# Kernel optimization log

Hardware: AMD Instinct MI355X
Metric: run time of the kernel (lower is better)

## Reference

```python
import jax, jax.numpy as jnp
import numpy as np

BIG_K, SMALL_K = 13, 3
NK = -(-BIG_K // SMALL_K)  # 5
NUM_PATHS = 3
BN_EPS = 1e-5


def _shifts():
    mid = BIG_K // 2
    pad = SMALL_K - 1
    return [-(mid - i * SMALL_K - pad) for i in range(NK)]  # [-4,-1,2,5,8]


def _conv1x1(x, w):
    return jax.lax.conv_general_dilated(
        x, w, window_strides=(1, 1), padding='VALID',
        dimension_numbers=('NCHW', 'OIHW', 'NCHW'))


def _dwconv3x3(x, w, groups):
    # x: (b, groups, h, w); w: (groups, 1, 3, 3)
    return jax.lax.conv_general_dilated(
        x, w, window_strides=(1, 1), padding=[(1, 1), (1, 1)],
        dimension_numbers=('NCHW', 'OIHW', 'NCHW'),
        feature_group_count=groups)


def setup_inputs() -> dict:
    key = jax.random.key(0)
    ks = jax.random.split(key, 8)
    b, c1, c2, h, w = 16, 256, 256, 64, 64
    return {
        'x': jax.random.normal(ks[0], (b, c1, h, w), jnp.float32),
        'w_expand': jax.random.normal(ks[1], (c2 * NK, c1, 1, 1), jnp.float32) * 0.05,
        'w_path': jax.random.normal(ks[2], (NUM_PATHS, NK, c2, 1, 3, 3), jnp.float32) * 0.1,
        'w_mix': jax.random.normal(ks[3], (c2, c2, 1, 1), jnp.float32) * 0.05,
        'bn_gamma': jnp.ones((c2,), jnp.float32),
        'bn_beta': jnp.zeros((c2,), jnp.float32),
        'bn_mean': jnp.zeros((c2,), jnp.float32),
        'bn_var': jnp.ones((c2,), jnp.float32),
    }


def reference(x, w_expand, w_path, w_mix, bn_gamma, bn_beta, bn_mean, bn_var):
    b, c1, h, w = x.shape
    c2 = w_mix.shape[0]
    # 1) channel expand: c1 -> c2*nk (1x1 conv, big GEMM)
    x_exp = _conv1x1(x, w_expand)                      # (b, c2*NK, h, w)
    x_r = x_exp.reshape(b, c2, NK, h, w)
    # 2) roll each shift group; conv is linear in kernel, so summing over the
    #    3 paths of depthwise weights gives identical math to summing outputs.
    shifts = _shifts()
    rolled = jnp.stack(
        [jnp.roll(x_r[:, :, k], (shifts[k], shifts[k]), axis=(2, 3)) for k in range(NK)],
        axis=2)                                        # (b, c2, NK, h, w)
    rolled_flat = rolled.reshape(b, c2 * NK, h, w)      # channel layout: c2-major, nk-minor
    w_eff = jnp.sum(w_path, axis=0)                     # (NK, c2, 1, 3, 3)
    w_flat = jnp.transpose(w_eff, (1, 0, 2, 3, 4)).reshape(c2 * NK, 1, 3, 3)
    conv_out = _dwconv3x3(rolled_flat, w_flat, groups=c2 * NK)
    merged = conv_out.reshape(b, c2, NK, h, w).sum(axis=2)  # sum over shifts (paths already folded)
    # 3) channel mix + BN (inference) + SiLU
    out = _conv1x1(merged, w_mix)
    inv = jax.lax.rsqrt(bn_var + BN_EPS)
    out = (out - bn_mean[None, :, None, None]) * (bn_gamma * inv)[None, :, None, None] + bn_beta[None, :, None, None]
    return out * jax.nn.sigmoid(out)  # SiLU
```

## Files before the change

kernel.cpp:

```cpp
#include <hip/hip_runtime.h>
#include <hip/hip_bf16.h>
#include <math.h>

#define NB   16
#define C1   256
#define C2   256
#define NK   5
#define NEXP (C2 * NK)
#define HW   4096

typedef __attribute__((ext_vector_type(8))) short bf16x8;
typedef __attribute__((ext_vector_type(4))) float f32x4;

#define GLOAD_LDS16(g, l) __builtin_amdgcn_global_load_lds( \
    (const __attribute__((address_space(1))) void*)(g), \
    (__attribute__((address_space(3))) void*)(l), 16, 0, 0)

__device__ __forceinline__ int bswz(int n, int kByte) {
    return n * 64 + (kByte ^ (((n >> 1) & 3) << 4));
}

__global__ void weff_kernel(const float* __restrict__ w_path, float* __restrict__ weff) {
    int idx = blockIdx.x * 256 + threadIdx.x;
    if (idx >= NK * C2 * 9) return;
    float s = 0.f;
    #pragma unroll
    for (int p = 0; p < 3; ++p)
        s += w_path[(long)p * NK * C2 * 9 + idx];
    weff[idx] = s;
}

__global__ void cvt_bf16_kernel(const float* __restrict__ in, __hip_bfloat16* __restrict__ out, int n) {
    int i = blockIdx.x * 256 + threadIdx.x;
    if (i < n) out[i] = __float2bfloat16(in[i]);
}

template <bool FP32B, bool OUT_BF16>
__global__ __launch_bounds__(256)
void gemm_mfma_kernel(const __hip_bfloat16* __restrict__ A,
                      const void* __restrict__ B_all,
                      void* __restrict__ C_all, int M, int N, int K,
                      long bStrideB, long bStrideC, int bOffB, int bOffC,
                      const float* __restrict__ bn_gamma, const float* __restrict__ bn_beta,
                      const float* __restrict__ bn_mean, const float* __restrict__ bn_var) {
    __shared__ __align__(16) short As[128 * 32];
    __shared__ __align__(16) short Bs[128 * 32];
    const int z = blockIdx.z;
    const int n0 = blockIdx.x * 128;
    const int m0 = blockIdx.y * 128;
    const int t = threadIdx.x;
    const int lane = t & 63;
    const int wid = t >> 6;
    const int wr = wid >> 1, wc = wid & 1;
    const int lr = lane & 15, lg = lane >> 4;
    const int sr = t >> 2;
    const int sc = (t & 3) * 8;

    const __hip_bfloat16* aP0 = &A[(long)(m0 + sr) * K + sc];
    const __hip_bfloat16* aP1 = &A[(long)(m0 + 64 + sr) * K + sc];
    short* aD0 = &As[sr * 32 + sc];
    short* aD1 = &As[(64 + sr) * 32 + sc];

    const int bn = t & 127;
    const int kg = t >> 7;
    const float* Bf = (const float*)B_all + (long)(bOffB + z) * bStrideB + n0 + bn;
    const short* Bh = (const short*)B_all + (long)(bOffB + z) * bStrideB + n0 + bn;
    char* bD0 = (char*)Bs + bswz(bn, kg * 32);
    char* bD1 = (char*)Bs + bswz(bn, kg * 32 + 16);

    int bOff[4];
    #pragma unroll
    for (int i = 0; i < 4; ++i)
        bOff[i] = bswz(wc * 64 + i * 16 + lr, lg * 16);

    f32x4 acc[4][4];
    #pragma unroll
    for (int i = 0; i < 4; ++i)
        #pragma unroll
        for (int j = 0; j < 4; ++j)
            acc[i][j] = (f32x4){0.f, 0.f, 0.f, 0.f};

    for (int k0 = 0; k0 < K; k0 += 32) {
        bf16x8 pk0, pk1;
        #pragma unroll
        for (int i = 0; i < 8; ++i) {
            if constexpr (FP32B) {
                float v0 = Bf[(long)(k0 + kg * 16 + i) * N];
                float v1 = Bf[(long)(k0 + kg * 16 + 8 + i) * N];
                __hip_bfloat16 h0 = __float2bfloat16(v0);
                __hip_bfloat16 h1 = __float2bfloat16(v1);
                pk0[i] = *reinterpret_cast<short*>(&h0);
                pk1[i] = *reinterpret_cast<short*>(&h1);
            } else {
                pk0[i] = Bh[(long)(k0 + kg * 16 + i) * N];
                pk1[i] = Bh[(long)(k0 + kg * 16 + 8 + i) * N];
            }
        }
        __syncthreads();
        GLOAD_LDS16(aP0 + k0, aD0);
        GLOAD_LDS16(aP1 + k0, aD1);
        *(bf16x8*)bD0 = pk0;
        *(bf16x8*)bD1 = pk1;
        __syncthreads();
        bf16x8 af[4], bfr[4];
        #pragma unroll
        for (int i = 0; i < 4; ++i) {
            af[i]  = *(const bf16x8*)&As[(wr * 64 + i * 16 + lr) * 32 + lg * 8];
            bfr[i] = *(const bf16x8*)((char*)Bs + bOff[i]);
        }
        #pragma unroll
        for (int i = 0; i < 4; ++i)
            #pragma unroll
            for (int j = 0; j < 4; ++j)
                acc[i][j] = __builtin_amdgcn_mfma_f32_16x16x32_bf16(af[i], bfr[j], acc[i][j], 0, 0, 0);
    }

    if constexpr (OUT_BF16) {
        __hip_bfloat16* C = (__hip_bfloat16*)C_all + (long)(bOffC + z) * bStrideC;
        #pragma unroll
        for (int i = 0; i < 4; ++i) {
            #pragma unroll
            for (int r = 0; r < 4; ++r) {
                long row = m0 + wr * 64 + i * 16 + lg * 4 + r;
                #pragma unroll
                for (int j = 0; j < 4; ++j)
                    C[row * N + n0 + wc * 64 + j * 16 + lr] = __float2bfloat16(acc[i][j][r]);
            }
        }
    } else {
        float* C = (float*)C_all + (long)(bOffC + z) * bStrideC;
        #pragma unroll
        for (int i = 0; i < 4; ++i) {
            #pragma unroll
            for (int r = 0; r < 4; ++r) {
                int row = m0 + wr * 64 + i * 16 + lg * 4 + r;
                float scale = bn_gamma[row] * rsqrtf(bn_var[row] + 1e-5f);
                float mn = bn_mean[row], bt = bn_beta[row];
                #pragma unroll
                for (int j = 0; j < 4; ++j) {
                    float v = (acc[i][j][r] - mn) * scale + bt;
                    C[(long)row * N + n0 + wc * 64 + j * 16 + lr] = v / (1.0f + __expf(-v));
                }
            }
        }
    }
}

__global__ __launch_bounds__(256)
void shift_dw_kernel(const __hip_bfloat16* __restrict__ xexp,
                     const float* __restrict__ weff,
                     __hip_bfloat16* __restrict__ merged) {
    __shared__ __align__(16) __hip_bfloat16 sd[NK * 34 * 64];
    const int t  = threadIdx.x;
    const int r0 = blockIdx.x * 32;
    const int c  = blockIdx.y;
    const int z  = blockIdx.z;
    const int shifts[NK] = {-4, -1, 2, 5, 8};
    const __hip_bfloat16* base = xexp + ((long)z * NEXP + (long)c * NK) * HW;

    for (int idx = t; idx < NK * 34 * 8; idx += 256) {
        int k   = idx / (34 * 8);
        int rem = idx - k * (34 * 8);
        int rr  = rem >> 3, ch = (rem & 7) * 8;
        int grow = (r0 - 1 + rr - shifts[k]) & 63;
        *(bf16x8*)&sd[(k * 34 + rr) * 64 + ch] =
            *(const bf16x8*)(base + (long)k * HW + grow * 64 + ch);
    }
    __syncthreads();

    const int j  = t & 63;
    const int ty = t >> 6;
    const int pbase = ty * 8;
    const bool topEdge = (r0 == 0)  && (ty == 0);
    const bool botEdge = (r0 == 32) && (ty == 3);

    float2 acc[4];
    #pragma unroll
    for (int i = 0; i < 4; ++i) acc[i] = (float2){0.f, 0.f};

    #pragma unroll
    for (int k = 0; k < NK; ++k) {
        const int s = shifts[k];
        const int cL = (j - 1 - s) & 63;
        const int cC = (j - s) & 63;
        const int cR = (j + 1 - s) & 63;
        const float* wp = &weff[((long)k * C2 + c) * 9];
        float w[9];
        #pragma unroll
        for (int i = 0; i < 9; ++i) w[i] = wp[i];
        if (j == 0)  { w[0] = 0.f; w[3] = 0.f; w[6] = 0.f; }
        if (j == 63) { w[2] = 0.f; w[5] = 0.f; w[8] = 0.f; }
        const __hip_bfloat16* pl = &sd[k * 34 * 64];

        float vL[4], vC[4], vR[4];
        #pragma unroll
        for (int w4 = 0; w4 < 4; ++w4) {
            vL[w4] = __bfloat162float(pl[(pbase + w4) * 64 + cL]);
            vC[w4] = __bfloat162float(pl[(pbase + w4) * 64 + cC]);
            vR[w4] = __bfloat162float(pl[(pbase + w4) * 64 + cR]);
        }
        if (topEdge) { vL[0] = 0.f; vC[0] = 0.f; vR[0] = 0.f; }

        #pragma unroll
        for (int pr = 0; pr < 4; ++pr) {
            #pragma unroll
            for (int u = 0; u < 3; ++u) {
                const int wi  = (2 * pr + u) & 3;
                const int wi2 = (2 * pr + u + 1) & 3;
                acc[pr].x += w[u*3+0] * vL[wi]  + w[u*3+1] * vC[wi]  + w[u*3+2] * vR[wi];
                acc[pr].y += w[u*3+0] * vL[wi2] + w[u*3+1] * vC[wi2] + w[u*3+2] * vR[wi2];
            }
            if (pr < 3) {
                const int na = (2 * pr) & 3, nb = (2 * pr + 1) & 3;
                const int ra = pbase + 2 * pr + 4, rb = pbase + 2 * pr + 5;
                vL[na] = __bfloat162float(pl[ra * 64 + cL]);
                vC[na] = __bfloat162float(pl[ra * 64 + cC]);
                vR[na] = __bfloat162float(pl[ra * 64 + cR]);
                vL[nb] = __bfloat162float(pl[rb * 64 + cL]);
                vC[nb] = __bfloat162float(pl[rb * 64 + cC]);
                vR[nb] = __bfloat162float(pl[rb * 64 + cR]);
                if (botEdge && pr == 2) { vL[nb] = 0.f; vC[nb] = 0.f; vR[nb] = 0.f; }
            }
        }
    }

    long outb = ((long)z * C2 + c) * HW + (long)(r0 + ty * 8) * 64 + j;
    #pragma unroll
    for (int pr = 0; pr < 4; ++pr) {
        merged[outb + (long)(2 * pr) * 64]     = __float2bfloat16(acc[pr].x);
        merged[outb + (long)(2 * pr + 1) * 64] = __float2bfloat16(acc[pr].y);
    }
}

extern "C" void kernel_launch(void* const* d_in, const int* in_sizes, int n_in,
                              void* d_out, int out_size, void* d_ws, size_t ws_size,
                              hipStream_t stream) {
    const float* x        = (const float*)d_in[0];
    const float* w_expand = (const float*)d_in[1];
    const float* w_path   = (const float*)d_in[2];
    const float* w_mix    = (const float*)d_in[3];
    const float* bn_gamma = (const float*)d_in[4];
    const float* bn_beta  = (const float*)d_in[5];
    const float* bn_mean  = (const float*)d_in[6];
    const float* bn_var   = (const float*)d_in[7];

    char* ws = (char*)d_ws;
    float* weff             = (float*)ws;
    __hip_bfloat16* wexp_bf = (__hip_bfloat16*)(ws + 65536);
    __hip_bfloat16* wmix_bf = (__hip_bfloat16*)(ws + 65536 + 655360);
    const size_t head = 1 << 20;

    const size_t xe_per = (size_t)NEXP * HW * 2;
    const size_t mg_per = (size_t)C2 * HW * 2;
    const size_t per_b = xe_per + mg_per;

    int g = 1;
    if (ws_size > head + per_b) {
        size_t fit = (ws_size - head) / per_b;
        g = (int)(fit < NB ? fit : NB);
        if (g < 1) g = 1;
    }

    char* p = ws + head;
    __hip_bfloat16* xexp   = (__hip_bfloat16*)p; p += (size_t)g * xe_per;
    __hip_bfloat16* merged = (__hip_bfloat16*)p;

    weff_kernel<<<(NK * C2 * 9 + 255) / 256, 256, 0, stream>>>(w_path, weff);
    cvt_bf16_kernel<<<(NEXP * C1 + 255) / 256, 256, 0, stream>>>(w_expand, wexp_bf, NEXP * C1);
    cvt_bf16_kernel<<<(C2 * C2 + 255) / 256, 256, 0, stream>>>(w_mix, wmix_bf, C2 * C2);

    for (int b0 = 0; b0 < NB; b0 += g) {
        int gb = (NB - b0) < g ? (NB - b0) : g;
        gemm_mfma_kernel<true, true><<<dim3(HW / 128, NEXP / 128, gb), 256, 0, stream>>>(
            wexp_bf, x, xexp, NEXP, HW, C1,
            (long)C1 * HW, (long)NEXP * HW, b0, 0,
            nullptr, nullptr, nullptr, nullptr);
        shift_dw_kernel<<<dim3(2, C2, gb), 256, 0, stream>>>(xexp, weff, merged);
        gemm_mfma_kernel<false, false><<<dim3(HW / 128, C2 / 128, gb), 256, 0, stream>>>(
            wmix_bf, merged, d_out, C2, HW, C2,
            (long)C2 * HW, (long)C2 * HW, 0, b0,
            bn_gamma, bn_beta, bn_mean, bn_var);
    }
}
```

Measured before the change: 248.2 us.

## Double-buffer GEMM LDS tiles, vectorize B loads and transpose MFMA output stores

The MFMA GEMM now keeps two LDS buffers so the next K-tile's global loads (A through direct-to-LDS, B through registers) are issued while the current tile is computed, needing one barrier per iteration instead of two. B is read with vectorized float4/bf16x8 loads and packed as k-pairs, and both tiles use an XOR swizzle to avoid LDS bank conflicts. The MFMA operands are swapped so each lane owns four consecutive columns, which lets the epilogue write short4/float4 vectors instead of scattered scalars. The cost is double the LDS footprint, which may lower occupancy, plus more complex swizzle indexing that has to stay correct.

```diff
diff --git a/kernel.cpp b/kernel.cpp
--- a/kernel.cpp
+++ b/kernel.cpp
@@ -16,8 +16,10 @@
     (const __attribute__((address_space(1))) void*)(g), \
     (__attribute__((address_space(3))) void*)(l), 16, 0, 0)
 
-__device__ __forceinline__ int bswz(int n, int kByte) {
-    return n * 64 + (kByte ^ (((n >> 1) & 3) << 4));
+__device__ __forceinline__ int swzkey(int r) { return ((r >> 1) & 3) ^ ((r >> 3) & 3); }
+
+__device__ __forceinline__ unsigned short bfbits(float v) {
+    return __builtin_bit_cast(unsigned short, __float2bfloat16(v));
 }
 
 __global__ void weff_kernel(const float* __restrict__ w_path, float* __restrict__ weff) {
@@ -43,8 +45,8 @@
                       long bStrideB, long bStrideC, int bOffB, int bOffC,
                       const float* __restrict__ bn_gamma, const float* __restrict__ bn_beta,
                       const float* __restrict__ bn_mean, const float* __restrict__ bn_var) {
-    __shared__ __align__(16) short As[128 * 32];
-    __shared__ __align__(16) short Bs[128 * 32];
+    __shared__ __align__(16) short As[2][128 * 32];
+    __shared__ __align__(16) short Bs[2][128 * 32];
     const int z = blockIdx.z;
     const int n0 = blockIdx.x * 128;
     const int m0 = blockIdx.y * 128;
@@ -53,25 +55,52 @@
     const int wid = t >> 6;
     const int wr = wid >> 1, wc = wid & 1;
     const int lr = lane & 15, lg = lane >> 4;
-    const int sr = t >> 2;
-    const int sc = (t & 3) * 8;
-
-    const __hip_bfloat16* aP0 = &A[(long)(m0 + sr) * K + sc];
-    const __hip_bfloat16* aP1 = &A[(long)(m0 + 64 + sr) * K + sc];
-    short* aD0 = &As[sr * 32 + sc];
-    short* aD1 = &As[(64 + sr) * 32 + sc];
-
-    const int bn = t & 127;
-    const int kg = t >> 7;
-    const float* Bf = (const float*)B_all + (long)(bOffB + z) * bStrideB + n0 + bn;
-    const short* Bh = (const short*)B_all + (long)(bOffB + z) * bStrideB + n0 + bn;
-    char* bD0 = (char*)Bs + bswz(bn, kg * 32);
-    char* bD1 = (char*)Bs + bswz(bn, kg * 32 + 16);
-
-    int bOff[4];
-    #pragma unroll
-    for (int i = 0; i < 4; ++i)
-        bOff[i] = bswz(wc * 64 + i * 16 + lr, lg * 16);
+
+    const int arow = t >> 2, achk = t & 3;
+    const int akey = swzkey(arow);
+    const __hip_bfloat16* aS0 = A + (long)(m0 + arow) * K + (achk ^ akey) * 8;
+    const __hip_bfloat16* aS1 = A + (long)(m0 + 64 + arow) * K + (achk ^ akey) * 8;
+
+    const int pr = (t >> 4) & 15;
+    const int ng = t & 15;
+    const char* Bbase = (const char*)B_all + (long)(bOffB + z) * bStrideB * (FP32B ? 4 : 2);
+
+    int bwoff[8];
+    #pragma unroll
+    for (int jj = 0; jj < 8; ++jj) {
+        int n = ng * 8 + jj;
+        bwoff[jj] = n * 64 + (((pr >> 2) ^ swzkey(n)) << 4) + (pr & 3) * 4;
+    }
+    int aroff[4], broff[4];
+    #pragma unroll
+    for (int i = 0; i < 4; ++i) {
+        int r = wr * 64 + i * 16 + lr;
+        aroff[i] = r * 64 + ((lg ^ swzkey(r)) << 4);
+        int n = wc * 64 + i * 16 + lr;
+        broff[i] = n * 64 + ((lg ^ swzkey(n)) << 4);
+    }
+
+    auto loadB = [&](int k0, unsigned u[8]) {
+        if constexpr (FP32B) {
+            const float* p0 = (const float*)Bbase + (long)(k0 + 2 * pr) * N + n0 + ng * 8;
+            const float* p1 = p0 + N;
+            float4 x0 = ((const float4*)p0)[0], x1 = ((const float4*)p0)[1];
+            float4 y0 = ((const float4*)p1)[0], y1 = ((const float4*)p1)[1];
+            float xs[8] = {x0.x, x0.y, x0.z, x0.w, x1.x, x1.y, x1.z, x1.w};
+            float ys[8] = {y0.x, y0.y, y0.z, y0.w, y1.x, y1.y, y1.z, y1.w};
+            #pragma unroll
+            for (int jj = 0; jj < 8; ++jj)
+                u[jj] = (unsigned)bfbits(xs[jj]) | ((unsigned)bfbits(ys[jj]) << 16);
+        } else {
+            const short* p0 = (const short*)Bbase + (long)(k0 + 2 * pr) * N + n0 + ng * 8;
+            bf16x8 r0 = *(const bf16x8*)p0;
+            bf16x8 r1 = *(const bf16x8*)(p0 + N);
+            #pragma unroll
+            for (int jj = 0; jj < 8; ++jj)
+                u[jj] = (unsigned)(unsigned short)r0[jj] |
+                        ((unsigned)(unsigned short)r1[jj] << 16);
+        }
+    };
 
     f32x4 acc[4][4];
     #pragma unroll
@@ -80,67 +109,82 @@
         for (int j = 0; j < 4; ++j)
             acc[i][j] = (f32x4){0.f, 0.f, 0.f, 0.f};
 
-    for (int k0 = 0; k0 < K; k0 += 32) {
-        bf16x8 pk0, pk1;
-        #pragma unroll
-        for (int i = 0; i < 8; ++i) {
-            if constexpr (FP32B) {
-                float v0 = Bf[(long)(k0 + kg * 16 + i) * N];
-                float v1 = Bf[(long)(k0 + kg * 16 + 8 + i) * N];
-                __hip_bfloat16 h0 = __float2bfloat16(v0);
-                __hip_bfloat16 h1 = __float2bfloat16(v1);
-                pk0[i] = *reinterpret_cast<short*>(&h0);
-                pk1[i] = *reinterpret_cast<short*>(&h1);
-            } else {
-                pk0[i] = Bh[(long)(k0 + kg * 16 + i) * N];
-                pk1[i] = Bh[(long)(k0 + kg * 16 + 8 + i) * N];
-            }
+    const int NT = K / 32;
+    unsigned ub[8];
+    loadB(0, ub);
+    GLOAD_LDS16(aS0, (char*)&As[0][0] + t * 16);
+    GLOAD_LDS16(aS1, (char*)&As[0][0] + 4096 + t * 16);
+    #pragma unroll
+    for (int jj = 0; jj < 8; ++jj)
+        *(unsigned*)((char*)&Bs[0][0] + bwoff[jj]) = ub[jj];
+    __syncthreads();
+
+    int buf = 0;
+    for (int it = 0; it < NT; ++it) {
+        unsigned un[8];
+        const bool more = (it + 1) < NT;
+        if (more) {
+            int k0 = (it + 1) * 32;
+            loadB(k0, un);
+            GLOAD_LDS16(aS0 + k0, (char*)&As[buf ^ 1][0] + t * 16);
+            GLOAD_LDS16(aS1 + k0, (char*)&As[buf ^ 1][0] + 4096 + t * 16);
+        }
+        bf16x8 af[4], bfr[4];
+        #pragma unroll
+        for (int i = 0; i < 4; ++i) {
+            af[i]  = *(const bf16x8*)((const char*)&As[buf][0] + aroff[i]);
+            bfr[i] = *(const bf16x8*)((const char*)&Bs[buf][0] + broff[i]);
+        }
+        #pragma unroll
+        for (int i = 0; i < 4; ++i)
+            #pragma unroll
+            for (int j = 0; j < 4; ++j)
+                acc[i][j] = __builtin_amdgcn_mfma_f32_16x16x32_bf16(bfr[j], af[i], acc[i][j], 0, 0, 0);
+        if (more) {
+            #pragma unroll
+            for (int jj = 0; jj < 8; ++jj)
+                *(unsigned*)((char*)&Bs[buf ^ 1][0] + bwoff[jj]) = un[jj];
         }
         __syncthreads();
-        GLOAD_LDS16(aP0 + k0, aD0);
-        GLOAD_LDS16(aP1 + k0, aD1);
-        *(bf16x8*)bD0 = pk0;
-        *(bf16x8*)bD1 = pk1;
-        __syncthreads();
-        bf16x8 af[4], bfr[4];
-        #pragma unroll
-        for (int i = 0; i < 4; ++i) {
-            af[i]  = *(const bf16x8*)&As[(wr * 64 + i * 16 + lr) * 32 + lg * 8];
-            bfr[i] = *(const bf16x8*)((char*)Bs + bOff[i]);
-        }
-        #pragma unroll
-        for (int i = 0; i < 4; ++i)
-            #pragma unroll
-            for (int j = 0; j < 4; ++j)
-                acc[i][j] = __builtin_amdgcn_mfma_f32_16x16x32_bf16(af[i], bfr[j], acc[i][j], 0, 0, 0);
+        buf ^= 1;
     }
 
     if constexpr (OUT_BF16) {
         __hip_bfloat16* C = (__hip_bfloat16*)C_all + (long)(bOffC + z) * bStrideC;
         #pragma unroll
         for (int i = 0; i < 4; ++i) {
-            #pragma unroll
-            for (int r = 0; r < 4; ++r) {
-                long row = m0 + wr * 64 + i * 16 + lg * 4 + r;
-                #pragma unroll
-                for (int j = 0; j < 4; ++j)
-                    C[row * N + n0 + wc * 64 + j * 16 + lr] = __float2bfloat16(acc[i][j][r]);
+            const int m = m0 + wr * 64 + i * 16 + lr;
+            #pragma unroll
+            for (int j = 0; j < 4; ++j) {
+                const long n = n0 + wc * 64 + j * 16 + lg * 4;
+                short4 sv;
+                sv.x = (short)bfbits(acc[i][j][0]);
+                sv.y = (short)bfbits(acc[i][j][1]);
+                sv.z = (short)bfbits(acc[i][j][2]);
+                sv.w = (short)bfbits(acc[i][j][3]);
+                *(short4*)(C + (long)m * N + n) = sv;
             }
         }
     } else {
         float* C = (float*)C_all + (long)(bOffC + z) * bStrideC;
         #pragma unroll
         for (int i = 0; i < 4; ++i) {
-            #pragma unroll
-            for (int r = 0; r < 4; ++r) {
-                int row = m0 + wr * 64 + i * 16 + lg * 4 + r;
-                float scale = bn_gamma[row] * rsqrtf(bn_var[row] + 1e-5f);
-                float mn = bn_mean[row], bt = bn_beta[row];
-                #pragma unroll
-                for (int j = 0; j < 4; ++j) {
-                    float v = (acc[i][j][r] - mn) * scale + bt;
-                    C[(long)row * N + n0 + wc * 64 + j * 16 + lr] = v / (1.0f + __expf(-v));
-                }
+            const int m = m0 + wr * 64 + i * 16 + lr;
+            const float scale = bn_gamma[m] * rsqrtf(bn_var[m] + 1e-5f);
+            const float mn = bn_mean[m], bt = bn_beta[m];
+            #pragma unroll
+            for (int j = 0; j < 4; ++j) {
+                const long n = n0 + wc * 64 + j * 16 + lg * 4;
+                float4 v;
+                float t0 = (acc[i][j][0] - mn) * scale + bt;
+                float t1 = (acc[i][j][1] - mn) * scale + bt;
+                float t2 = (acc[i][j][2] - mn) * scale + bt;
+                float t3 = (acc[i][j][3] - mn) * scale + bt;
+                v.x = t0 / (1.0f + __expf(-t0));
+                v.y = t1 / (1.0f + __expf(-t1));
+                v.z = t2 / (1.0f + __expf(-t2));
+                v.w = t3 / (1.0f + __expf(-t3));
+                *(float4*)(C + (long)m * N + n) = v;
             }
         }
     }
```

After: 265.6 us. 7.0% more time.

## Rewrite 1x1-conv GEMMs with register-resident weights and full-K B tile in LDS

Applied to the files above, without the earlier changes.

Replaces the K-looped 128x128 GEMM with a 512-thread kernel specialised for K=256. Each wave keeps its 32 weight rows for the whole K in registers, and the block stages the entire 256x128 activation tile in XOR-swizzled LDS once, so there is no per-k-step synchronisation. Operands are swapped so the output is vector-stored along N, using short4/float4 stores instead of scalar ones. This trades occupancy (64KB LDS, launch bounds of one block, heavy register use) for fewer barriers and wider stores.

```diff
diff --git a/kernel.cpp b/kernel.cpp
--- a/kernel.cpp
+++ b/kernel.cpp
@@ -12,12 +12,8 @@
 typedef __attribute__((ext_vector_type(8))) short bf16x8;
 typedef __attribute__((ext_vector_type(4))) float f32x4;
 
-#define GLOAD_LDS16(g, l) __builtin_amdgcn_global_load_lds( \
-    (const __attribute__((address_space(1))) void*)(g), \
-    (__attribute__((address_space(3))) void*)(l), 16, 0, 0)
-
-__device__ __forceinline__ int bswz(int n, int kByte) {
-    return n * 64 + (kByte ^ (((n >> 1) & 3) << 4));
+__device__ __forceinline__ unsigned short bfbits(float v) {
+    return __builtin_bit_cast(unsigned short, __float2bfloat16(v));
 }
 
 __global__ void weff_kernel(const float* __restrict__ w_path, float* __restrict__ weff) {
@@ -36,111 +32,113 @@
 }
 
 template <bool FP32B, bool OUT_BF16>
-__global__ __launch_bounds__(256)
-void gemm_mfma_kernel(const __hip_bfloat16* __restrict__ A,
-                      const void* __restrict__ B_all,
-                      void* __restrict__ C_all, int M, int N, int K,
-                      long bStrideB, long bStrideC, int bOffB, int bOffC,
-                      const float* __restrict__ bn_gamma, const float* __restrict__ bn_beta,
-                      const float* __restrict__ bn_mean, const float* __restrict__ bn_var) {
-    __shared__ __align__(16) short As[128 * 32];
-    __shared__ __align__(16) short Bs[128 * 32];
-    const int z = blockIdx.z;
+__global__ __launch_bounds__(512, 1)
+void ws_gemm_kernel(const __hip_bfloat16* __restrict__ A,
+                    const void* __restrict__ B_all,
+                    void* __restrict__ C_all,
+                    long bStrideB, long bStrideC, int bOffB, int bOffC,
+                    const float* __restrict__ bn_gamma, const float* __restrict__ bn_beta,
+                    const float* __restrict__ bn_mean, const float* __restrict__ bn_var) {
+    constexpr int KK = 256, NN = 4096;
+    __shared__ __align__(16) char Bs[128 * 512];
+    const int z  = blockIdx.z;
     const int n0 = blockIdx.x * 128;
-    const int m0 = blockIdx.y * 128;
-    const int t = threadIdx.x;
+    const int m0 = blockIdx.y * 256;
+    const int t  = threadIdx.x;
     const int lane = t & 63;
-    const int wid = t >> 6;
-    const int wr = wid >> 1, wc = wid & 1;
+    const int wv = t >> 6;
     const int lr = lane & 15, lg = lane >> 4;
-    const int sr = t >> 2;
-    const int sc = (t & 3) * 8;
-
-    const __hip_bfloat16* aP0 = &A[(long)(m0 + sr) * K + sc];
-    const __hip_bfloat16* aP1 = &A[(long)(m0 + 64 + sr) * K + sc];
-    short* aD0 = &As[sr * 32 + sc];
-    short* aD1 = &As[(64 + sr) * 32 + sc];
-
-    const int bn = t & 127;
-    const int kg = t >> 7;
-    const float* Bf = (const float*)B_all + (long)(bOffB + z) * bStrideB + n0 + bn;
-    const short* Bh = (const short*)B_all + (long)(bOffB + z) * bStrideB + n0 + bn;
-    char* bD0 = (char*)Bs + bswz(bn, kg * 32);
-    char* bD1 = (char*)Bs + bswz(bn, kg * 32 + 16);
-
-    int bOff[4];
-    #pragma unroll
-    for (int i = 0; i < 4; ++i)
-        bOff[i] = bswz(wc * 64 + i * 16 + lr, lg * 16);
-
-    f32x4 acc[4][4];
-    #pragma unroll
-    for (int i = 0; i < 4; ++i)
-        #pragma unroll
-        for (int j = 0; j < 4; ++j)
-            acc[i][j] = (f32x4){0.f, 0.f, 0.f, 0.f};
-
-    for (int k0 = 0; k0 < K; k0 += 32) {
-        bf16x8 pk0, pk1;
-        #pragma unroll
-        for (int i = 0; i < 8; ++i) {
-            if constexpr (FP32B) {
-                float v0 = Bf[(long)(k0 + kg * 16 + i) * N];
-                float v1 = Bf[(long)(k0 + kg * 16 + 8 + i) * N];
-                __hip_bfloat16 h0 = __float2bfloat16(v0);
-                __hip_bfloat16 h1 = __float2bfloat16(v1);
-                pk0[i] = *reinterpret_cast<short*>(&h0);
-                pk1[i] = *reinterpret_cast<short*>(&h1);
-            } else {
-                pk0[i] = Bh[(long)(k0 + kg * 16 + i) * N];
-                pk1[i] = Bh[(long)(k0 + kg * 16 + 8 + i) * N];
-            }
-        }
-        __syncthreads();
-        GLOAD_LDS16(aP0 + k0, aD0);
-        GLOAD_LDS16(aP1 + k0, aD1);
-        *(bf16x8*)bD0 = pk0;
-        *(bf16x8*)bD1 = pk1;
-        __syncthreads();
-        bf16x8 af[4], bfr[4];
-        #pragma unroll
-        for (int i = 0; i < 4; ++i) {
-            af[i]  = *(const bf16x8*)&As[(wr * 64 + i * 16 + lr) * 32 + lg * 8];
-            bfr[i] = *(const bf16x8*)((char*)Bs + bOff[i]);
-        }
-        #pragma unroll
-        for (int i = 0; i < 4; ++i)
-            #pragma unroll
-            for (int j = 0; j < 4; ++j)
-                acc[i][j] = __builtin_amdgcn_mfma_f32_16x16x32_bf16(af[i], bfr[j], acc[i][j], 0, 0, 0);
+
+    bf16x8 af[2][8];
+    const __hip_bfloat16* wp = A + (long)(m0 + wv * 32 + lr) * KK + lg * 8;
+    #pragma unroll
+    for (int s = 0; s < 2; ++s)
+        #pragma unroll
+        for (int ks = 0; ks < 8; ++ks)
+            af[s][ks] = *(const bf16x8*)(wp + (long)s * 16 * KK + ks * 32);
+
+    const int sn = t & 127;
+    const int kb = (t >> 7) * 64;
+    const int key = sn & 31;
+    const char* Bbase = (const char*)B_all + (long)(bOffB + z) * bStrideB * (FP32B ? 4 : 2);
+    #pragma unroll
+    for (int gq = 0; gq < 4; ++gq) {
+        unsigned u[8];
+        if constexpr (FP32B) {
+            const float* p = (const float*)Bbase + (long)(kb + gq * 16) * NN + n0 + sn;
+            #pragma unroll
+            for (int i = 0; i < 8; ++i) {
+                float v0 = p[(long)(2 * i) * NN];
+                float v1 = p[(long)(2 * i + 1) * NN];
+                u[i] = (unsigned)bfbits(v0) | ((unsigned)bfbits(v1) << 16);
+            }
+        } else {
+            const unsigned short* p = (const unsigned short*)Bbase + (long)(kb + gq * 16) * NN + n0 + sn;
+            #pragma unroll
+            for (int i = 0; i < 8; ++i)
+                u[i] = (unsigned)p[(long)(2 * i) * NN] |
+                       ((unsigned)p[(long)(2 * i + 1) * NN] << 16);
+        }
+        const int ch0 = kb / 8 + gq * 2;
+        *(uint4*)(Bs + sn * 512 + ((ch0 ^ key) * 16))       = *(uint4*)&u[0];
+        *(uint4*)(Bs + sn * 512 + (((ch0 + 1) ^ key) * 16)) = *(uint4*)&u[4];
+    }
+    __syncthreads();
+
+    f32x4 acc[2][8];
+    #pragma unroll
+    for (int s = 0; s < 2; ++s)
+        #pragma unroll
+        for (int j = 0; j < 8; ++j)
+            acc[s][j] = (f32x4){0.f, 0.f, 0.f, 0.f};
+
+    #pragma unroll
+    for (int ks = 0; ks < 8; ++ks) {
+        #pragma unroll
+        for (int j = 0; j < 8; ++j) {
+            const int n = j * 16 + lr;
+            bf16x8 bfr = *(const bf16x8*)(Bs + n * 512 + (((ks * 4 + lg) ^ (n & 31)) * 16));
+            acc[0][j] = __builtin_amdgcn_mfma_f32_16x16x32_bf16(bfr, af[0][ks], acc[0][j], 0, 0, 0);
+            acc[1][j] = __builtin_amdgcn_mfma_f32_16x16x32_bf16(bfr, af[1][ks], acc[1][j], 0, 0, 0);
+        }
     }
 
     if constexpr (OUT_BF16) {
         __hip_bfloat16* C = (__hip_bfloat16*)C_all + (long)(bOffC + z) * bStrideC;
         #pragma unroll
-        for (int i = 0; i < 4; ++i) {
-            #pragma unroll
-            for (int r = 0; r < 4; ++r) {
-                long row = m0 + wr * 64 + i * 16 + lg * 4 + r;
-                #pragma unroll
-                for (int j = 0; j < 4; ++j)
-                    C[row * N + n0 + wc * 64 + j * 16 + lr] = __float2bfloat16(acc[i][j][r]);
+        for (int s = 0; s < 2; ++s) {
+            const int m = m0 + wv * 32 + s * 16 + lr;
+            #pragma unroll
+            for (int j = 0; j < 8; ++j) {
+                const long n = n0 + j * 16 + lg * 4;
+                short4 sv;
+                sv.x = (short)bfbits(acc[s][j][0]);
+                sv.y = (short)bfbits(acc[s][j][1]);
+                sv.z = (short)bfbits(acc[s][j][2]);
+                sv.w = (short)bfbits(acc[s][j][3]);
+                *(short4*)(C + (long)m * NN + n) = sv;
             }
         }
     } else {
         float* C = (float*)C_all + (long)(bOffC + z) * bStrideC;
         #pragma unroll
-        for (int i = 0; i < 4; ++i) {
-            #pragma unroll
-            for (int r = 0; r < 4; ++r) {
-                int row = m0 + wr * 64 + i * 16 + lg * 4 + r;
-                float scale = bn_gamma[row] * rsqrtf(bn_var[row] + 1e-5f);
-                float mn = bn_mean[row], bt = bn_beta[row];
-                #pragma unroll
-                for (int j = 0; j < 4; ++j) {
-                    float v = (acc[i][j][r] - mn) * scale + bt;
-                    C[(long)row * N + n0 + wc * 64 + j * 16 + lr] = v / (1.0f + __expf(-v));
-                }
+        for (int s = 0; s < 2; ++s) {
+            const int m = m0 + wv * 32 + s * 16 + lr;
+            const float scale = bn_gamma[m] * rsqrtf(bn_var[m] + 1e-5f);
+            const float mn = bn_mean[m], bt = bn_beta[m];
+            #pragma unroll
+            for (int j = 0; j < 8; ++j) {
+                const long n = n0 + j * 16 + lg * 4;
+                float4 v;
+                float t0 = (acc[s][j][0] - mn) * scale + bt;
+                float t1 = (acc[s][j][1] - mn) * scale + bt;
+                float t2 = (acc[s][j][2] - mn) * scale + bt;
+                float t3 = (acc[s][j][3] - mn) * scale + bt;
+                v.x = t0 / (1.0f + __expf(-t0));
+                v.y = t1 / (1.0f + __expf(-t1));
+                v.z = t2 / (1.0f + __expf(-t2));
+                v.w = t3 / (1.0f + __expf(-t3));
+                *(float4*)(C + (long)m * NN + n) = v;
             }
         }
     }
@@ -271,13 +269,13 @@
 
     for (int b0 = 0; b0 < NB; b0 += g) {
         int gb = (NB - b0) < g ? (NB - b0) : g;
-        gemm_mfma_kernel<true, true><<<dim3(HW / 128, NEXP / 128, gb), 256, 0, stream>>>(
-            wexp_bf, x, xexp, NEXP, HW, C1,
+        ws_gemm_kernel<true, true><<<dim3(HW / 128, NEXP / 256, gb), 512, 0, stream>>>(
+            wexp_bf, x, xexp,
             (long)C1 * HW, (long)NEXP * HW, b0, 0,
             nullptr, nullptr, nullptr, nullptr);
         shift_dw_kernel<<<dim3(2, C2, gb), 256, 0, stream>>>(xexp, weff, merged);
-        gemm_mfma_kernel<false, false><<<dim3(HW / 128, C2 / 128, gb), 256, 0, stream>>>(
-            wmix_bf, merged, d_out, C2, HW, C2,
+        ws_gemm_kernel<false, false><<<dim3(HW / 128, 1, gb), 512, 0, stream>>>(
+            wmix_bf, merged, d_out,
             (long)C2 * HW, (long)C2 * HW, 0, b0,
             bn_gamma, bn_beta, bn_mean, bn_var);
     }
```

Result: slower. 258.3 us (+4.1%).
